# Performance work log

Measured on AMD Instinct MI355X. Metric: run time of the kernel, lower is better.

Reference implementation:

```python
import jax, jax.numpy as jnp
import numpy as np

B, NP, NG = 4, 8192, 8192

def setup_inputs() -> dict:
    key = jax.random.key(0)
    k1, k2, k3 = jax.random.split(key, 3)
    pr_pts = jax.random.normal(k1, (B, NP, 3), dtype=jnp.float32)
    gt_pts = jax.random.normal(k2, (B, NG, 3), dtype=jnp.float32)
    gt_valid = jax.random.randint(k3, (B, NG), 0, 2) > 0
    return {"pr_pts": pr_pts, "gt_pts": gt_pts, "gt_valid": gt_valid}

def _sq_dists(a, b):
    # a: [B,N,3], b: [B,M,3] -> squared pairwise distances [B,N,M]
    a2 = jnp.sum(a * a, -1)  # [B,N]
    b2 = jnp.sum(b * b, -1)  # [B,M]
    ab = jnp.einsum('bnd,bmd->bnm', a, b)
    return a2[:, :, None] + b2[:, None, :] - 2.0 * ab

def reference(pr_pts, gt_pts, gt_valid):
    # Bidirectional Chamfer distance with gt validity mask.
    d2 = _sq_dists(pr_pts, gt_pts)  # [B,Np,Ng]
    # accuracy: for each predicted point, min squared dist to a VALID gt point
    d2_masked = jnp.where(gt_valid[:, None, :], d2, jnp.inf)
    acc_b = jnp.mean(jnp.min(d2_masked, axis=-1), axis=-1)  # [B]
    # completeness: for each valid gt point, min squared dist to any pred point
    min_over_pr = jnp.min(d2, axis=1)  # [B,Ng]
    valid_f = gt_valid.astype(min_over_pr.dtype)
    com_b = jnp.sum(min_over_pr * valid_f, axis=-1) / jnp.maximum(jnp.sum(valid_f, axis=-1), 1.0)
    loss_acc = jnp.mean(acc_b)
    loss_com = jnp.mean(com_b)
    loss_cd = loss_acc + loss_com
    # Sum((loss_acc,None),(loss_com,None),(loss_cd,None)) with scalar losses -> acc+com+cd
    return loss_acc + loss_com + loss_cd
```

## Files before the change

### kernel.cpp

```cpp
#include <hip/hip_runtime.h>

#define BB 4
#define NN 8192

typedef _Float16 f16;
typedef _Float16 f16x8 __attribute__((ext_vector_type(8)));
typedef float f32x16 __attribute__((ext_vector_type(16)));

#define SZ_PACK (BB * NN * 16)
#define OFF_PART_BYTES (4 * SZ_PACK * 2)

__global__ __launch_bounds__(256) void k_init(
    const float* __restrict__ pr, const float* __restrict__ gt,
    const int* __restrict__ valid,
    f16* __restrict__ APR, f16* __restrict__ BGT,
    f16* __restrict__ AGT, f16* __restrict__ BPR) {
  int i = blockIdx.x * 256 + threadIdx.x;
  if (i >= BB * NN) return;
  float px = pr[3 * i], py = pr[3 * i + 1], pz = pr[3 * i + 2];
  float gx = gt[3 * i], gy = gt[3 * i + 1], gz = gt[3 * i + 2];
  int vld = valid[i] != 0;

  f16 phx = (f16)px, phy = (f16)py, phz = (f16)pz;
  f16 plx = (f16)(px - (float)phx), ply = (f16)(py - (float)phy), plz = (f16)(pz - (float)phz);
  float p2 = px * px + py * py + pz * pz;
  f16 p2h = (f16)p2, p2l = (f16)(p2 - (float)p2h);

  f16 ghx = (f16)gx, ghy = (f16)gy, ghz = (f16)gz;
  f16 glx = (f16)(gx - (float)ghx), gly = (f16)(gy - (float)ghy), glz = (f16)(gz - (float)ghz);
  float g2 = gx * gx + gy * gy + gz * gz;
  f16 g2h = (f16)g2, g2l = (f16)(g2 - (float)g2h);
  f16 g2hm = vld ? g2h : (f16)32768.0f;
  f16 g2lm = vld ? g2l : (f16)0.0f;

  const f16 one = (f16)1.0f, zero = (f16)0.0f;
  union Rec { f16 h[16]; uint4 u[2]; };

  Rec ra;
  ra.h[0] = (f16)(-2.f * (float)phx); ra.h[1] = (f16)(-2.f * (float)phy); ra.h[2] = (f16)(-2.f * (float)phz);
  ra.h[3] = ra.h[0]; ra.h[4] = ra.h[1]; ra.h[5] = ra.h[2];
  ra.h[6] = (f16)(-2.f * (float)plx); ra.h[7] = (f16)(-2.f * (float)ply); ra.h[8] = (f16)(-2.f * (float)plz);
  ra.h[9] = p2h; ra.h[10] = p2l; ra.h[11] = one; ra.h[12] = one;
  ra.h[13] = zero; ra.h[14] = zero; ra.h[15] = zero;
  ((uint4*)APR)[2 * i] = ra.u[0]; ((uint4*)APR)[2 * i + 1] = ra.u[1];

  Rec rb;
  rb.h[0] = phx; rb.h[1] = phy; rb.h[2] = phz;
  rb.h[3] = plx; rb.h[4] = ply; rb.h[5] = plz;
  rb.h[6] = phx; rb.h[7] = phy; rb.h[8] = phz;
  rb.h[9] = one; rb.h[10] = one; rb.h[11] = p2h; rb.h[12] = p2l;
  rb.h[13] = zero; rb.h[14] = zero; rb.h[15] = zero;
  ((uint4*)BPR)[2 * i] = rb.u[0]; ((uint4*)BPR)[2 * i + 1] = rb.u[1];

  Rec rc;
  rc.h[0] = (f16)(-2.f * (float)ghx); rc.h[1] = (f16)(-2.f * (float)ghy); rc.h[2] = (f16)(-2.f * (float)ghz);
  rc.h[3] = rc.h[0]; rc.h[4] = rc.h[1]; rc.h[5] = rc.h[2];
  rc.h[6] = (f16)(-2.f * (float)glx); rc.h[7] = (f16)(-2.f * (float)gly); rc.h[8] = (f16)(-2.f * (float)glz);
  rc.h[9] = g2h; rc.h[10] = g2l; rc.h[11] = one; rc.h[12] = one;
  rc.h[13] = zero; rc.h[14] = zero; rc.h[15] = zero;
  ((uint4*)AGT)[2 * i] = rc.u[0]; ((uint4*)AGT)[2 * i + 1] = rc.u[1];

  Rec rd;
  rd.h[0] = ghx; rd.h[1] = ghy; rd.h[2] = ghz;
  rd.h[3] = glx; rd.h[4] = gly; rd.h[5] = glz;
  rd.h[6] = ghx; rd.h[7] = ghy; rd.h[8] = ghz;
  rd.h[9] = one; rd.h[10] = one; rd.h[11] = g2hm; rd.h[12] = g2lm;
  rd.h[13] = zero; rd.h[14] = zero; rd.h[15] = zero;
  ((uint4*)BGT)[2 * i] = rd.u[0]; ((uint4*)BGT)[2 * i + 1] = rd.u[1];
}

__global__ __launch_bounds__(256, 4) void k_dist(
    const f16* __restrict__ APR, const f16* __restrict__ BGT,
    const f16* __restrict__ AGT, const f16* __restrict__ BPR,
    float* __restrict__ partial) {
  __shared__ f16 lds[2 * 1024 * 8];
  int id = blockIdx.x;
  int wgrow = id & 63;
  int half  = (id >> 6) & 1;
  int b     = (id >> 7) & 3;
  int p     = id >> 9;
  const f16* A  = p ? AGT : APR;
  const f16* Bv = p ? BPR : BGT;
  int tid = threadIdx.x;
  int wave = tid >> 6, lane = tid & 63;
  int nn = lane & 31, q = lane >> 5;

  const f16* Ab = A + ((size_t)b * NN + wgrow * 128 + wave * 32 + nn) * 16 + q * 8;
  f16x8 af = *(const f16x8*)Ab;

  f32x16 zc = {};
  f32x16 m;
#pragma unroll
  for (int i = 0; i < 16; ++i) m[i] = 1e38f;

  const uint4* gsrc = (const uint4*)(Bv + ((size_t)b * NN + half * 4096) * 16);
  uint4* ldsu = (uint4*)lds;
  const f16x8* lf = (const f16x8*)lds;

  for (int chunk = 0; chunk < 4; ++chunk) {
    const uint4* src = gsrc + (size_t)chunk * 2048;
#pragma unroll
    for (int k = 0; k < 8; ++k) {
      int u = tid + 256 * k;
      uint4 v = src[u];
      ldsu[(u & 1) * 1024 + (u >> 1)] = v;
    }
    __syncthreads();
#pragma unroll 8
    for (int t = 0; t < 32; ++t) {
      f16x8 bf = lf[q * 1024 + t * 32 + nn];
      f32x16 d = __builtin_amdgcn_mfma_f32_32x32x16_f16(af, bf, zc, 0, 0, 0);
#pragma unroll
      for (int i = 0; i < 16; ++i) m[i] = fminf(m[i], d[i]);
    }
    __syncthreads();
  }

#pragma unroll
  for (int i = 0; i < 16; ++i) {
    float v = m[i];
    v = fminf(v, __shfl_xor(v, 1, 64));
    v = fminf(v, __shfl_xor(v, 2, 64));
    v = fminf(v, __shfl_xor(v, 4, 64));
    v = fminf(v, __shfl_xor(v, 8, 64));
    v = fminf(v, __shfl_xor(v, 16, 64));
    m[i] = fmaxf(v, 0.0f);
  }

  float* pb = partial + (((size_t)(p * 4 + b) * 2 + half) * NN) + wgrow * 128 + wave * 32;
#pragma unroll
  for (int reg = 0; reg < 16; ++reg) {
    int rit = (reg & 3) + 8 * (reg >> 2) + 4 * q;
    if ((lane & 31) == reg) pb[rit] = m[reg];
  }
}

__global__ __launch_bounds__(1024) void k_red(
    const float* __restrict__ partial, const int* __restrict__ valid,
    float* __restrict__ out) {
  int tid = threadIdx.x;
  float sA[4] = {0, 0, 0, 0}, sC[4] = {0, 0, 0, 0}, sN[4] = {0, 0, 0, 0};
#pragma unroll
  for (int g = 0; g < 8; ++g) {
    int pp = g >> 2, bb = g & 3;
    const float* pb = partial + (size_t)g * 2 * NN;
    for (int r = tid; r < NN; r += 1024) {
      float v = fminf(pb[r], pb[NN + r]);
      if (pp == 0) {
        sA[bb] += v;
      } else {
        int vld = valid[bb * NN + r] != 0;
        sC[bb] += vld ? v : 0.0f;
        sN[bb] += vld ? 1.0f : 0.0f;
      }
    }
  }
  float vals[12] = {sA[0], sA[1], sA[2], sA[3], sC[0], sC[1], sC[2], sC[3],
                    sN[0], sN[1], sN[2], sN[3]};
  __shared__ float red[16][12];
  int wave = tid >> 6, lane = tid & 63;
#pragma unroll
  for (int k = 0; k < 12; ++k) {
    float v = vals[k];
    v += __shfl_xor(v, 1, 64);
    v += __shfl_xor(v, 2, 64);
    v += __shfl_xor(v, 4, 64);
    v += __shfl_xor(v, 8, 64);
    v += __shfl_xor(v, 16, 64);
    v += __shfl_xor(v, 32, 64);
    if (lane == 0) red[wave][k] = v;
  }
  __syncthreads();
  if (tid == 0) {
    float a = 0.f, c = 0.f;
    for (int bb = 0; bb < 4; ++bb) {
      float tA = 0.f, tC = 0.f, tN = 0.f;
      for (int w = 0; w < 16; ++w) {
        tA += red[w][bb]; tC += red[w][4 + bb]; tN += red[w][8 + bb];
      }
      a += tA / (float)NN;
      c += tC / fmaxf(tN, 1.0f);
    }
    out[0] = 0.5f * (a + c);
  }
}

extern "C" void kernel_launch(void* const* d_in, const int* in_sizes, int n_in,
                              void* d_out, int out_size, void* d_ws, size_t ws_size,
                              hipStream_t stream) {
  const float* pr    = (const float*)d_in[0];
  const float* gt    = (const float*)d_in[1];
  const int*   valid = (const int*)d_in[2];

  f16* base = (f16*)d_ws;
  f16* APR = base;
  f16* BGT = base + SZ_PACK;
  f16* AGT = base + 2 * SZ_PACK;
  f16* BPR = base + 3 * SZ_PACK;
  float* partial = (float*)((char*)d_ws + OFF_PART_BYTES);

  k_init<<<(BB * NN) / 256, 256, 0, stream>>>(pr, gt, valid, APR, BGT, AGT, BPR);
  k_dist<<<1024, 256, 0, stream>>>(APR, BGT, AGT, BPR, partial);
  k_red<<<1, 1024, 0, stream>>>(partial, valid, (float*)d_out);
}
```

Before: 108.0 us.

## Parallelize final reduction across blocks with atomics and pair MFMAs in distance loop

```diff
diff --git a/kernel.cpp b/kernel.cpp
--- a/kernel.cpp
+++ b/kernel.cpp
@@ -9,13 +9,16 @@
 
 #define SZ_PACK (BB * NN * 16)
 #define OFF_PART_BYTES (4 * SZ_PACK * 2)
+#define OFF_RES_BYTES (OFF_PART_BYTES + 16 * NN * 4)
 
 __global__ __launch_bounds__(256) void k_init(
     const float* __restrict__ pr, const float* __restrict__ gt,
     const int* __restrict__ valid,
     f16* __restrict__ APR, f16* __restrict__ BGT,
-    f16* __restrict__ AGT, f16* __restrict__ BPR) {
+    f16* __restrict__ AGT, f16* __restrict__ BPR,
+    float* __restrict__ res) {
   int i = blockIdx.x * 256 + threadIdx.x;
+  if (blockIdx.x == 0 && threadIdx.x < 16) res[threadIdx.x] = 0.0f;
   if (i >= BB * NN) return;
   float px = pr[3 * i], py = pr[3 * i + 1], pz = pr[3 * i + 2];
   float gx = gt[3 * i], gy = gt[3 * i + 1], gz = gt[3 * i + 2];
@@ -102,16 +105,17 @@
 #pragma unroll
     for (int k = 0; k < 8; ++k) {
       int u = tid + 256 * k;
-      uint4 v = src[u];
-      ldsu[(u & 1) * 1024 + (u >> 1)] = v;
+      ldsu[(u & 1) * 1024 + (u >> 1)] = src[u];
     }
     __syncthreads();
-#pragma unroll 8
-    for (int t = 0; t < 32; ++t) {
-      f16x8 bf = lf[q * 1024 + t * 32 + nn];
-      f32x16 d = __builtin_amdgcn_mfma_f32_32x32x16_f16(af, bf, zc, 0, 0, 0);
-#pragma unroll
-      for (int i = 0; i < 16; ++i) m[i] = fminf(m[i], d[i]);
+    for (int t = 0; t < 32; t += 2) {
+      f16x8 b0 = lf[q * 1024 + t * 32 + nn];
+      f16x8 b1 = lf[q * 1024 + (t + 1) * 32 + nn];
+      f32x16 d0 = __builtin_amdgcn_mfma_f32_32x32x16_f16(af, b0, zc, 0, 0, 0);
+      f32x16 d1 = __builtin_amdgcn_mfma_f32_32x32x16_f16(af, b1, zc, 0, 0, 0);
+#pragma unroll
+      for (int i = 0; i < 16; ++i)
+        m[i] = fminf(fminf(d0[i], d1[i]), m[i]);
     }
     __syncthreads();
   }
@@ -135,51 +139,50 @@
   }
 }
 
-__global__ __launch_bounds__(1024) void k_red(
+__global__ __launch_bounds__(256) void k_red(
     const float* __restrict__ partial, const int* __restrict__ valid,
-    float* __restrict__ out) {
+    float* __restrict__ res) {
+  int g = blockIdx.x >> 3, seg = blockIdx.x & 7;
+  int pp = g >> 2, bb = g & 3;
   int tid = threadIdx.x;
-  float sA[4] = {0, 0, 0, 0}, sC[4] = {0, 0, 0, 0}, sN[4] = {0, 0, 0, 0};
-#pragma unroll
-  for (int g = 0; g < 8; ++g) {
-    int pp = g >> 2, bb = g & 3;
-    const float* pb = partial + (size_t)g * 2 * NN;
-    for (int r = tid; r < NN; r += 1024) {
-      float v = fminf(pb[r], pb[NN + r]);
-      if (pp == 0) {
-        sA[bb] += v;
-      } else {
-        int vld = valid[bb * NN + r] != 0;
-        sC[bb] += vld ? v : 0.0f;
-        sN[bb] += vld ? 1.0f : 0.0f;
-      }
-    }
-  }
-  float vals[12] = {sA[0], sA[1], sA[2], sA[3], sC[0], sC[1], sC[2], sC[3],
-                    sN[0], sN[1], sN[2], sN[3]};
-  __shared__ float red[16][12];
-  int wave = tid >> 6, lane = tid & 63;
-#pragma unroll
-  for (int k = 0; k < 12; ++k) {
-    float v = vals[k];
-    v += __shfl_xor(v, 1, 64);
-    v += __shfl_xor(v, 2, 64);
-    v += __shfl_xor(v, 4, 64);
-    v += __shfl_xor(v, 8, 64);
-    v += __shfl_xor(v, 16, 64);
-    v += __shfl_xor(v, 32, 64);
-    if (lane == 0) red[wave][k] = v;
-  }
+  const float* pb = partial + (size_t)g * 2 * NN;
+
+  float sum = 0.0f, cnt = 0.0f;
+#pragma unroll
+  for (int k = 0; k < 4; ++k) {
+    int r = seg * 1024 + tid + 256 * k;
+    float v = fminf(pb[r], pb[NN + r]);
+    if (pp == 0) {
+      sum += v;
+    } else {
+      int vld = valid[bb * NN + r] != 0;
+      sum += vld ? v : 0.0f;
+      cnt += vld ? 1.0f : 0.0f;
+    }
+  }
+  __shared__ float r1[256], r2[256];
+  r1[tid] = sum; r2[tid] = cnt;
   __syncthreads();
+  for (int off = 128; off > 0; off >>= 1) {
+    if (tid < off) { r1[tid] += r1[tid + off]; r2[tid] += r2[tid + off]; }
+    __syncthreads();
+  }
   if (tid == 0) {
+    if (pp == 0) {
+      atomicAdd(&res[bb], r1[0]);
+    } else {
+      atomicAdd(&res[4 + bb], r1[0]);
+      atomicAdd(&res[8 + bb], r2[0]);
+    }
+  }
+}
+
+__global__ void k_final(const float* __restrict__ res, float* __restrict__ out) {
+  if (threadIdx.x == 0 && blockIdx.x == 0) {
     float a = 0.f, c = 0.f;
     for (int bb = 0; bb < 4; ++bb) {
-      float tA = 0.f, tC = 0.f, tN = 0.f;
-      for (int w = 0; w < 16; ++w) {
-        tA += red[w][bb]; tC += red[w][4 + bb]; tN += red[w][8 + bb];
-      }
-      a += tA / (float)NN;
-      c += tC / fmaxf(tN, 1.0f);
+      a += res[bb] / (float)NN;
+      c += res[4 + bb] / fmaxf(res[8 + bb], 1.0f);
     }
     out[0] = 0.5f * (a + c);
   }
@@ -198,8 +201,10 @@
   f16* AGT = base + 2 * SZ_PACK;
   f16* BPR = base + 3 * SZ_PACK;
   float* partial = (float*)((char*)d_ws + OFF_PART_BYTES);
-
-  k_init<<<(BB * NN) / 256, 256, 0, stream>>>(pr, gt, valid, APR, BGT, AGT, BPR);
+  float* res     = (float*)((char*)d_ws + OFF_RES_BYTES);
+
+  k_init<<<(BB * NN) / 256, 256, 0, stream>>>(pr, gt, valid, APR, BGT, AGT, BPR, res);
   k_dist<<<1024, 256, 0, stream>>>(APR, BGT, AGT, BPR, partial);
-  k_red<<<1, 1024, 0, stream>>>(partial, valid, (float*)d_out);
-}
+  k_red<<<64, 256, 0, stream>>>(partial, valid, res);
+  k_final<<<1, 64, 0, stream>>>(res, (float*)d_out);
+}
```

Result: faster. 89.84 us (-16.9%).
